# Kernel tuning notes

Hardware: AMD Instinct MI355X
Metric: run time of the kernel (lower is better)

Reference implementation:

```python
import jax, jax.numpy as jnp
import numpy as np

B, T, C, I = 4, 4096, 1024, 4096

def rmsnorm(x, w, eps=1e-6):
    return x * jax.lax.rsqrt(jnp.mean(x * x, axis=-1, keepdims=True) + eps) * w

def shift(h):
    # prepend zeros, drop last timestep: (B,T,C)
    return jnp.pad(h, ((0, 0), (1, 0), (0, 0)))[:, :-1]

def wkv_scan(k, v, w, u):
    # k, v: (B,T,C) fp32; w, u: (C,)
    ew = jnp.exp(jnp.clip(w, -20.0, 20.0))
    def step(carry, kv):
        a, b = carry
        kt, vt = kv  # (B,C)
        ekt = jnp.exp(jnp.clip(u + kt, -20.0, 20.0))
        out = (a + ekt * vt) / (b + ekt + 1e-8)
        ek = jnp.exp(jnp.clip(kt, -20.0, 20.0))
        return (ew * a + ek * vt, ew * b + ek), out
    init = (jnp.zeros((k.shape[0], k.shape[2]), jnp.float32),
            jnp.zeros((k.shape[0], k.shape[2]), jnp.float32))
    _, out = jax.lax.scan(step, init, (k.swapaxes(0, 1), v.swapaxes(0, 1)))
    return out.swapaxes(0, 1)  # (B,T,C)

def setup_inputs() -> dict:
    key = jax.random.key(0)
    ks = jax.random.split(key, 16)
    s = 1.0 / np.sqrt(C)
    si = 1.0 / np.sqrt(I)
    return {
        "x": jax.random.normal(ks[0], (B, T, C), jnp.float32),
        "ln1_w": jnp.ones((C,), jnp.float32),
        "ln2_w": jnp.ones((C,), jnp.float32),
        "time_decay": jax.random.normal(ks[1], (C,), jnp.float32) * 0.1 - 5.0,
        "time_first": jax.random.normal(ks[2], (C,), jnp.float32) * 0.01,
        "time_mix_k": jnp.full((C,), 0.5, jnp.float32),
        "time_mix_v": jnp.full((C,), 0.5, jnp.float32),
        "time_mix_r": jnp.full((C,), 0.5, jnp.float32),
        "W_key": jax.random.normal(ks[3], (C, C), jnp.float32) * s,
        "W_value": jax.random.normal(ks[4], (C, C), jnp.float32) * s,
        "W_recept": jax.random.normal(ks[5], (C, C), jnp.float32) * s,
        "W_out": jax.random.normal(ks[6], (C, C), jnp.float32) * s,
        "time_mix_k2": jnp.full((C,), 0.5, jnp.float32),
        "time_mix_r2": jnp.full((C,), 0.5, jnp.float32),
        "W_key2": jax.random.normal(ks[7], (C, I), jnp.float32) * s,
        "W_value2": jax.random.normal(ks[8], (I, C), jnp.float32) * si,
        "W_recept2": jax.random.normal(ks[9], (C, C), jnp.float32) * s,
    }

def reference(x, ln1_w, ln2_w, time_decay, time_first,
              time_mix_k, time_mix_v, time_mix_r,
              W_key, W_value, W_recept, W_out,
              time_mix_k2, time_mix_r2, W_key2, W_value2, W_recept2):
    # --- time mixing ---
    h = rmsnorm(x, ln1_w)
    sh = shift(h)
    xk = h * time_mix_k + sh * (1 - time_mix_k)
    xv = h * time_mix_v + sh * (1 - time_mix_v)
    xr = h * time_mix_r + sh * (1 - time_mix_r)
    k = xk @ W_key
    v = xv @ W_value
    r = jax.nn.sigmoid(xr @ W_recept)
    w = -jnp.exp(time_decay)
    u = time_first
    wkv = wkv_scan(k.astype(jnp.float32), v.astype(jnp.float32), w, u).astype(x.dtype)
    x = x + (r * wkv) @ W_out
    # --- channel mixing ---
    h = rmsnorm(x, ln2_w)
    sh = shift(h)
    xk = h * time_mix_k2 + sh * (1 - time_mix_k2)
    xr = h * time_mix_r2 + sh * (1 - time_mix_r2)
    k2 = jnp.square(jax.nn.relu(xk @ W_key2))
    r2 = jax.nn.sigmoid(xr @ W_recept2)
    return x + r2 * (k2 @ W_value2)
```

## Files before the change

kernel.cpp:

```cpp
#include <hip/hip_runtime.h>
#include <cstdint>
#include <cstddef>

#define B_ 4
#define T_ 4096
#define C_ 1024
#define I_ 4096
#define M_ (B_*T_)

__device__ __forceinline__ float bf2f(uint16_t u) {
    union { uint32_t i; float f; } v; v.i = ((uint32_t)u) << 16; return v.f;
}
__device__ __forceinline__ uint16_t f2bf(float f) {
    union { float f; uint32_t i; } v; v.f = f;
    uint32_t i = v.i;
    return (uint16_t)((i + 0x7fffu + ((i >> 16) & 1u)) >> 16);
}

typedef __bf16 bf16x8 __attribute__((ext_vector_type(8)));
typedef float  f32x4  __attribute__((ext_vector_type(4)));

__device__ __forceinline__ void async16(const void* g, void* l) {
    __builtin_amdgcn_global_load_lds(
        (const __attribute__((address_space(1))) void*)g,
        (__attribute__((address_space(3))) void*)l, 16, 0, 0);
}

__global__ void sniff_kernel(const uint32_t* __restrict__ w,
                             int* __restrict__ flag, int* __restrict__ one) {
    *flag = (w[0] == 0x3F003F00u) ? 1 : 0;
    *one = 1;
}

struct VecPtrs { const void* s[9]; uint16_t* d[9]; };
__global__ __launch_bounds__(256) void convert_vecs(VecPtrs p, const int* __restrict__ flagp) {
    const int f = *flagp;
    const int tid = threadIdx.x;
    for (int a = 0; a < 9; ++a) {
        const void* s = p.s[a]; uint16_t* d = p.d[a];
        for (int i = tid; i < C_; i += 256)
            d[i] = f ? ((const uint16_t*)s)[i] : f2bf(((const float*)s)[i]);
    }
}

struct TJobs { const void* src[7]; uint16_t* dst[7]; };
__global__ __launch_bounds__(256) void transpose_all(TJobs tj, const int* __restrict__ flagp)
{
    __shared__ uint16_t tile[64][65];
    const int f = *flagp;
    const int bid = blockIdx.x;
    int w, t, R, Cc, cx, cy;
    if (bid < 1280) {
        w = bid >> 8; t = bid & 255; R = C_; Cc = C_; cx = t & 15; cy = t >> 4;
    } else if (bid < 2304) {
        w = 5; t = bid - 1280; R = C_; Cc = I_; cx = t & 63; cy = t >> 6;
    } else {
        w = 6; t = bid - 2304; R = I_; Cc = C_; cx = t & 15; cy = t >> 4;
    }
    const void* in = tj.src[w];
    uint16_t* out = tj.dst[w];
    const int lc = threadIdx.x & 63;
    const int rg = threadIdx.x >> 6;
    const int c0 = cx * 64, r0 = cy * 64;
    #pragma unroll
    for (int i = 0; i < 16; ++i) {
        int lr = rg * 16 + i;
        size_t idx = (size_t)(r0 + lr) * Cc + c0 + lc;
        tile[lr][lc] = f ? ((const uint16_t*)in)[idx] : f2bf(((const float*)in)[idx]);
    }
    __syncthreads();
    #pragma unroll
    for (int i = 0; i < 16; ++i) {
        int lcc = rg * 16 + i;
        out[(size_t)(c0 + lcc) * R + r0 + lc] = tile[lc][lcc];
    }
}

__global__ __launch_bounds__(256) void mix_kernel(
    const void* __restrict__ x, const uint16_t* __restrict__ ln,
    const uint16_t* __restrict__ mk, const uint16_t* __restrict__ mv,
    const uint16_t* __restrict__ mr, const int* __restrict__ flagp,
    uint16_t* __restrict__ xk, uint16_t* __restrict__ xv, uint16_t* __restrict__ xr)
{
    const int row = blockIdx.x;
    const int tid = threadIdx.x;
    const int f = *flagp;
    const bool hasPrev = (row & (T_ - 1)) != 0;
    const size_t base = (size_t)row * C_;

    float c[4], p[4];
    if (f) {
        const uint16_t* xb = (const uint16_t*)x;
        uint2 cu = ((const uint2*)(xb + base))[tid];
        uint2 pu; pu.x = 0u; pu.y = 0u;
        if (hasPrev) pu = ((const uint2*)(xb + base - C_))[tid];
        c[0] = bf2f((uint16_t)(cu.x & 0xffff)); c[1] = bf2f((uint16_t)(cu.x >> 16));
        c[2] = bf2f((uint16_t)(cu.y & 0xffff)); c[3] = bf2f((uint16_t)(cu.y >> 16));
        p[0] = bf2f((uint16_t)(pu.x & 0xffff)); p[1] = bf2f((uint16_t)(pu.x >> 16));
        p[2] = bf2f((uint16_t)(pu.y & 0xffff)); p[3] = bf2f((uint16_t)(pu.y >> 16));
    } else {
        const float* xf = (const float*)x;
        float4 cf = ((const float4*)(xf + base))[tid];
        float4 pf; pf.x = pf.y = pf.z = pf.w = 0.f;
        if (hasPrev) pf = ((const float4*)(xf + base - C_))[tid];
        c[0] = cf.x; c[1] = cf.y; c[2] = cf.z; c[3] = cf.w;
        p[0] = pf.x; p[1] = pf.y; p[2] = pf.z; p[3] = pf.w;
    }

    float s1 = c[0]*c[0] + c[1]*c[1] + c[2]*c[2] + c[3]*c[3];
    float s2 = p[0]*p[0] + p[1]*p[1] + p[2]*p[2] + p[3]*p[3];
    #pragma unroll
    for (int off = 32; off > 0; off >>= 1) {
        s1 += __shfl_down(s1, off);
        s2 += __shfl_down(s2, off);
    }
    __shared__ float red[8];
    const int lane = tid & 63, wave = tid >> 6;
    if (lane == 0) { red[wave * 2] = s1; red[wave * 2 + 1] = s2; }
    __syncthreads();
    s1 = red[0] + red[2] + red[4] + red[6];
    s2 = red[1] + red[3] + red[5] + red[7];
    const float rs1 = rsqrtf(s1 * (1.f / C_) + 1e-6f);
    const float rs2 = rsqrtf(s2 * (1.f / C_) + 1e-6f);

    uint2 lnu = ((const uint2*)ln)[tid];
    uint2 mku = ((const uint2*)mk)[tid];
    uint2 mru = ((const uint2*)mr)[tid];
    float lnv[4] = { bf2f((uint16_t)(lnu.x & 0xffff)), bf2f((uint16_t)(lnu.x >> 16)),
                     bf2f((uint16_t)(lnu.y & 0xffff)), bf2f((uint16_t)(lnu.y >> 16)) };
    float mkv[4] = { bf2f((uint16_t)(mku.x & 0xffff)), bf2f((uint16_t)(mku.x >> 16)),
                     bf2f((uint16_t)(mku.y & 0xffff)), bf2f((uint16_t)(mku.y >> 16)) };
    float mrv[4] = { bf2f((uint16_t)(mru.x & 0xffff)), bf2f((uint16_t)(mru.x >> 16)),
                     bf2f((uint16_t)(mru.y & 0xffff)), bf2f((uint16_t)(mru.y >> 16)) };

    float h[4], sh[4];
    #pragma unroll
    for (int e = 0; e < 4; ++e) {
        h[e]  = c[e] * rs1 * lnv[e];
        sh[e] = p[e] * rs2 * lnv[e];
    }

    uint16_t ok[4], orr[4];
    #pragma unroll
    for (int e = 0; e < 4; ++e) {
        ok[e]  = f2bf(h[e] * mkv[e] + sh[e] * (1.f - mkv[e]));
        orr[e] = f2bf(h[e] * mrv[e] + sh[e] * (1.f - mrv[e]));
    }
    uint2 w;
    w.x = (uint32_t)ok[0] | ((uint32_t)ok[1] << 16);  w.y = (uint32_t)ok[2] | ((uint32_t)ok[3] << 16);
    ((uint2*)(xk + base))[tid] = w;
    w.x = (uint32_t)orr[0] | ((uint32_t)orr[1] << 16); w.y = (uint32_t)orr[2] | ((uint32_t)orr[3] << 16);
    ((uint2*)(xr + base))[tid] = w;

    if (xv != nullptr) {
        uint2 mvu = ((const uint2*)mv)[tid];
        float mvv[4] = { bf2f((uint16_t)(mvu.x & 0xffff)), bf2f((uint16_t)(mvu.x >> 16)),
                         bf2f((uint16_t)(mvu.y & 0xffff)), bf2f((uint16_t)(mvu.y >> 16)) };
        uint16_t ov[4];
        #pragma unroll
        for (int e = 0; e < 4; ++e)
            ov[e] = f2bf(h[e] * mvv[e] + sh[e] * (1.f - mvv[e]));
        w.x = (uint32_t)ov[0] | ((uint32_t)ov[1] << 16);  w.y = (uint32_t)ov[2] | ((uint32_t)ov[3] << 16);
        ((uint2*)(xv + base))[tid] = w;
    }
}

#define SCAN_L   64
#define SCAN_NCH (T_ / SCAN_L)

__global__ __launch_bounds__(256) void wkv_pass1(
    const uint16_t* __restrict__ kb, const uint16_t* __restrict__ vb,
    const uint16_t* __restrict__ td,
    float* __restrict__ sumA, float* __restrict__ sumB)
{
    const int gid = blockIdx.x * 256 + threadIdx.x;
    const int c = gid & (C_ - 1);
    const int j = (gid >> 10) & (SCAN_NCH - 1);
    const int b = gid >> 16;
    float w = -__expf(bf2f(td[c]));
    w = fminf(fmaxf(w, -20.f), 20.f);
    const float ew = __expf(w);
    const size_t base = ((size_t)(b * T_ + j * SCAN_L)) * C_ + c;
    float A = 0.f, Bs = 0.f;
    #pragma unroll 8
    for (int i = 0; i < SCAN_L; ++i) {
        float kt = bf2f(kb[base + (size_t)i * C_]);
        float vt = bf2f(vb[base + (size_t)i * C_]);
        float ek = __expf(fminf(fmaxf(kt, -20.f), 20.f));
        A  = ew * A  + ek * vt;
        Bs = ew * Bs + ek;
    }
    const size_t sidx = ((size_t)(b * SCAN_NCH + j)) * C_ + c;
    sumA[sidx] = A; sumB[sidx] = Bs;
}

__global__ __launch_bounds__(256) void wkv_pass2(
    const float* __restrict__ sumA, const float* __restrict__ sumB,
    const uint16_t* __restrict__ td,
    float* __restrict__ a0s, float* __restrict__ b0s)
{
    const int gid = blockIdx.x * 256 + threadIdx.x;
    const int c = gid & (C_ - 1);
    const int b = gid >> 10;
    float w = -__expf(bf2f(td[c]));
    w = fminf(fmaxf(w, -20.f), 20.f);
    const float dL = __expf(w * (float)SCAN_L);
    float a = 0.f, bs = 0.f;
    for (int j = 0; j < SCAN_NCH; ++j) {
        size_t idx = ((size_t)(b * SCAN_NCH + j)) * C_ + c;
        a0s[idx] = a; b0s[idx] = bs;
        a  = dL * a  + sumA[idx];
        bs = dL * bs + sumB[idx];
    }
}

__global__ __launch_bounds__(256) void wkv_pass3(
    const uint16_t* __restrict__ kb, const uint16_t* __restrict__ vb,
    const uint16_t* __restrict__ rb, const uint16_t* __restrict__ td,
    const uint16_t* __restrict__ tf,
    const float* __restrict__ a0s, const float* __restrict__ b0s,
    uint16_t* __restrict__ rwkv)
{
    const int gid = blockIdx.x * 256 + threadIdx.x;
    const int c = gid & (C_ - 1);
    const int j = (gid >> 10) & (SCAN_NCH - 1);
    const int b = gid >> 16;
    float w = -__expf(bf2f(td[c]));
    w = fminf(fmaxf(w, -20.f), 20.f);
    const float ew = __expf(w);
    const float u = bf2f(tf[c]);
    const size_t base = ((size_t)(b * T_ + j * SCAN_L)) * C_ + c;
    const size_t sidx = ((size_t)(b * SCAN_NCH + j)) * C_ + c;
    float a = a0s[sidx], bs = b0s[sidx];
    #pragma unroll 4
    for (int i = 0; i < SCAN_L; ++i) {
        float kt = bf2f(kb[base + (size_t)i * C_]);
        float vt = bf2f(vb[base + (size_t)i * C_]);
        float rt = bf2f(rb[base + (size_t)i * C_]);
        float eu = __expf(fminf(fmaxf(u + kt, -20.f), 20.f));
        float out = __fdividef(a + eu * vt, bs + eu + 1e-8f);
        rwkv[base + (size_t)i * C_] = f2bf(rt * out);
        float ek = __expf(fminf(fmaxf(kt, -20.f), 20.f));
        a  = ew * a  + ek * vt;
        bs = ew * bs + ek;
    }
}

struct GJob {
    const uint16_t* A; const uint16_t* BT; void* Out;
    const void* aux1; const uint16_t* aux2;
    int mode; int N; int K;
};
struct GJobs { GJob j[3]; };

#define EP_PITCH 72
#define EP_QUAD  4608

__global__ __launch_bounds__(256) void gemm_rt(GJobs js, const int* __restrict__ flagp)
{
    __shared__ uint16_t smem[18432];
    uint16_t* sA = smem;
    uint16_t* sB = smem + 8192;

    const GJob jb = js.j[blockIdx.z];
    const int N = jb.N, K = jb.K, mode = jb.mode;
    const int tid = threadIdx.x;
    const int lane = tid & 63, wave = tid >> 6;
    const int wr = wave >> 1, wc = wave & 1;
    const int laneM = lane & 15, quad = lane >> 4;

    const int pid = blockIdx.y * gridDim.x + blockIdx.x;
    const int group_size = 16 * gridDim.x;
    const int grp = pid / group_size;
    const int sub = pid - grp * group_size;
    const int pm = grp * 16 + (sub & 15);
    const int pn = sub >> 4;
    if (pn * 128 >= N) return;
    const int tileM = pm * 128, tileN = pn * 128;

    int f = 1;
    if (mode == 2 || mode == 4) f = *flagp;

    f32x4 acc[4][4];
    #pragma unroll
    for (int i = 0; i < 4; ++i)
        #pragma unroll
        for (int j = 0; j < 4; ++j)
            acc[i][j] = (f32x4){0.f, 0.f, 0.f, 0.f};

    const uint16_t* Abase = jb.A  + (size_t)tileM * K;
    const uint16_t* Bbase = jb.BT + (size_t)tileN * K;

    int srow[4], scol[4];
    #pragma unroll
    for (int it = 0; it < 4; ++it) {
        int g = it * 256 + tid;
        srow[it] = g >> 3;
        scol[it] = ((g & 7) ^ (srow[it] & 7)) * 8;
    }
    const int swz = laneM & 7;

    for (int kt = 0; kt < K; kt += 64) {
        #pragma unroll
        for (int it = 0; it < 4; ++it)
            async16(Abase + (size_t)srow[it] * K + kt + scol[it], &sA[(it * 256 + tid) * 8]);
        #pragma unroll
        for (int it = 0; it < 4; ++it)
            async16(Bbase + (size_t)srow[it] * K + kt + scol[it], &sB[(it * 256 + tid) * 8]);
        __syncthreads();
        #pragma unroll
        for (int h = 0; h < 2; ++h) {
            bf16x8 av[4], bv[4];
            const int gk = (h * 4 + quad) ^ swz;
            #pragma unroll
            for (int i = 0; i < 4; ++i) {
                av[i] = *(const bf16x8*)&sA[(wr * 64 + i * 16 + laneM) * 64 + gk * 8];
                bv[i] = *(const bf16x8*)&sB[(wc * 64 + i * 16 + laneM) * 64 + gk * 8];
            }
            #pragma unroll
            for (int i = 0; i < 4; ++i)
                #pragma unroll
                for (int j = 0; j < 4; ++j)
                    acc[i][j] = __builtin_amdgcn_mfma_f32_16x16x32_bf16(av[i], bv[j], acc[i][j], 0, 0, 0);
        }
        __syncthreads();
    }

    const int qbase = (wr * 2 + wc) * EP_QUAD;
    #pragma unroll
    for (int i = 0; i < 4; ++i) {
        #pragma unroll
        for (int j = 0; j < 4; ++j) {
            #pragma unroll
            for (int rr = 0; rr < 4; ++rr) {
                float v = acc[i][j][rr];
                if (mode == 1) v = __fdividef(1.f, 1.f + __expf(-v));
                else if (mode == 3) { float t = fmaxf(v, 0.f); v = t * t; }
                int row_l = i * 16 + quad * 4 + rr;
                int col_l = j * 16 + laneM;
                smem[qbase + row_l * EP_PITCH + col_l] = f2bf(v);
            }
        }
    }
    __syncthreads();

    #pragma unroll
    for (int s = 0; s < 8; ++s) {
        int segid = s * 256 + tid;
        int gr = segid >> 4;
        int c0 = (segid & 15) * 8;
        int lidx = ((gr >> 6) * 2 + (c0 >> 6)) * EP_QUAD + (gr & 63) * EP_PITCH + (c0 & 63);
        uint4 pk = *(const uint4*)&smem[lidx];
        size_t idx = (size_t)(tileM + gr) * N + tileN + c0;

        if (mode == 0 || mode == 1 || mode == 3) {
            *(uint4*)((uint16_t*)jb.Out + idx) = pk;
        } else {
            union { uint4 u; uint16_t h[8]; } P; P.u = pk;
            float vals[8];
            #pragma unroll
            for (int e = 0; e < 8; ++e) vals[e] = bf2f(P.h[e]);
            if (mode == 2) {
                float xres[8];
                if (f) {
                    union { uint4 u; uint16_t h[8]; } A1;
                    A1.u = *(const uint4*)((const uint16_t*)jb.aux1 + idx);
                    #pragma unroll
                    for (int e = 0; e < 8; ++e) xres[e] = bf2f(A1.h[e]);
                } else {
                    const float* af = (const float*)jb.aux1 + idx;
                    float4 a0 = *(const float4*)af;
                    float4 a1 = *(const float4*)(af + 4);
                    xres[0]=a0.x; xres[1]=a0.y; xres[2]=a0.z; xres[3]=a0.w;
                    xres[4]=a1.x; xres[5]=a1.y; xres[6]=a1.z; xres[7]=a1.w;
                }
                union { uint4 u; uint16_t h[8]; } O;
                #pragma unroll
                for (int e = 0; e < 8; ++e) O.h[e] = f2bf(vals[e] + xres[e]);
                *(uint4*)((uint16_t*)jb.Out + idx) = O.u;
            } else {
                union { uint4 u; uint16_t h[8]; } A1, A2;
                A1.u = *(const uint4*)((const uint16_t*)jb.aux1 + idx);
                A2.u = *(const uint4*)(jb.aux2 + idx);
                float res[8];
                #pragma unroll
                for (int e = 0; e < 8; ++e)
                    res[e] = bf2f(A1.h[e]) + bf2f(A2.h[e]) * vals[e];
                if (f) {
                    union { uint4 u; uint16_t h[8]; } O;
                    #pragma unroll
                    for (int e = 0; e < 8; ++e) O.h[e] = f2bf(res[e]);
                    *(uint4*)((uint16_t*)jb.Out + idx) = O.u;
                } else {
                    float* of = (float*)jb.Out + idx;
                    *(float4*)of       = (float4){res[0], res[1], res[2], res[3]};
                    *(float4*)(of + 4) = (float4){res[4], res[5], res[6], res[7]};
                }
            }
        }
    }
}

extern "C" void kernel_launch(void* const* d_in, const int* in_sizes, int n_in,
                              void* d_out, int out_size, void* d_ws, size_t ws_size,
                              hipStream_t stream)
{
    const void* x   = d_in[0];
    const void* ln1 = d_in[1];
    const void* ln2 = d_in[2];
    const void* td  = d_in[3];
    const void* tf  = d_in[4];
    const void* mk  = d_in[5];
    const void* mv  = d_in[6];
    const void* mr  = d_in[7];
    const void* Wk  = d_in[8];
    const void* Wv  = d_in[9];
    const void* Wr  = d_in[10];
    const void* Wo  = d_in[11];
    const void* mk2 = d_in[12];
    const void* mr2 = d_in[13];
    const void* Wk2 = d_in[14];
    const void* Wv2 = d_in[15];
    const void* Wr2 = d_in[16];

    char* ws = (char*)d_ws;
    const size_t MiB = 1u << 20;
    uint16_t* WkT  = (uint16_t*)(ws + 0 * MiB);
    uint16_t* WvT  = (uint16_t*)(ws + 2 * MiB);
    uint16_t* WrT  = (uint16_t*)(ws + 4 * MiB);
    uint16_t* WoT  = (uint16_t*)(ws + 6 * MiB);
    uint16_t* Wr2T = (uint16_t*)(ws + 8 * MiB);
    uint16_t* Wk2T = (uint16_t*)(ws + 10 * MiB);
    uint16_t* Wv2T = (uint16_t*)(ws + 18 * MiB);
    uint16_t* A0 = (uint16_t*)(ws + 26 * MiB);
    uint16_t* A1 = (uint16_t*)(ws + 58 * MiB);
    uint16_t* A2 = (uint16_t*)(ws + 90 * MiB);
    uint16_t* A3 = (uint16_t*)(ws + 122 * MiB);
    uint16_t* A4 = (uint16_t*)(ws + 154 * MiB);
    uint16_t* A5 = (uint16_t*)(ws + 186 * MiB);
    uint16_t* k2 = (uint16_t*)(ws + 122 * MiB);
    float* sumA = (float*)(ws + 58 * MiB);
    float* sumB = (float*)(ws + 59 * MiB);
    float* a0s  = (float*)(ws + 60 * MiB);
    float* b0s  = (float*)(ws + 61 * MiB);
    int* flagp = (int*)(ws + 250 * MiB);
    int* onep  = (int*)(ws + 250 * MiB + 16);
    uint16_t* vecs = (uint16_t*)(ws + 250 * MiB + 64);
    uint16_t* ln1c = vecs + 0 * C_;
    uint16_t* ln2c = vecs + 1 * C_;
    uint16_t* tdc  = vecs + 2 * C_;
    uint16_t* tfc  = vecs + 3 * C_;
    uint16_t* mkc  = vecs + 4 * C_;
    uint16_t* mvc  = vecs + 5 * C_;
    uint16_t* mrc  = vecs + 6 * C_;
    uint16_t* mk2c = vecs + 7 * C_;
    uint16_t* mr2c = vecs + 8 * C_;

    uint16_t* xk   = A0;
    uint16_t* xv   = A1;
    uint16_t* xr   = A2;
    uint16_t* kb   = A3;
    uint16_t* vb   = A4;
    uint16_t* rb   = A5;
    uint16_t* rwkv = A0;
    uint16_t* x2   = A1;
    uint16_t* xk2  = A2;
    uint16_t* xr2  = A3;
    uint16_t* r2   = A0;

    dim3 blk(256);

    sniff_kernel<<<1, 1, 0, stream>>>((const uint32_t*)mk, flagp, onep);
    VecPtrs vp;
    vp.s[0] = ln1; vp.s[1] = ln2; vp.s[2] = td;  vp.s[3] = tf;  vp.s[4] = mk;
    vp.s[5] = mv;  vp.s[6] = mr;  vp.s[7] = mk2; vp.s[8] = mr2;
    vp.d[0] = ln1c; vp.d[1] = ln2c; vp.d[2] = tdc;  vp.d[3] = tfc;  vp.d[4] = mkc;
    vp.d[5] = mvc;  vp.d[6] = mrc;  vp.d[7] = mk2c; vp.d[8] = mr2c;
    convert_vecs<<<1, blk, 0, stream>>>(vp, flagp);

    TJobs tj;
    tj.src[0] = Wk;  tj.dst[0] = WkT;
    tj.src[1] = Wv;  tj.dst[1] = WvT;
    tj.src[2] = Wr;  tj.dst[2] = WrT;
    tj.src[3] = Wo;  tj.dst[3] = WoT;
    tj.src[4] = Wr2; tj.dst[4] = Wr2T;
    tj.src[5] = Wk2; tj.dst[5] = Wk2T;
    tj.src[6] = Wv2; tj.dst[6] = Wv2T;
    transpose_all<<<3328, blk, 0, stream>>>(tj, flagp);

    mix_kernel<<<M_, blk, 0, stream>>>(x, ln1c, mkc, mvc, mrc, flagp, xk, xv, xr);

    GJobs kvr;
    kvr.j[0] = GJob{ xk, WkT, kb, nullptr, nullptr, 0, C_, C_ };
    kvr.j[1] = GJob{ xv, WvT, vb, nullptr, nullptr, 0, C_, C_ };
    kvr.j[2] = GJob{ xr, WrT, rb, nullptr, nullptr, 1, C_, C_ };
    gemm_rt<<<dim3(C_ / 128, M_ / 128, 3), blk, 0, stream>>>(kvr, flagp);

    wkv_pass1<<<(B_ * SCAN_NCH * C_) / 256, blk, 0, stream>>>(kb, vb, tdc, sumA, sumB);
    wkv_pass2<<<(B_ * C_) / 256, blk, 0, stream>>>(sumA, sumB, tdc, a0s, b0s);
    wkv_pass3<<<(B_ * SCAN_NCH * C_) / 256, blk, 0, stream>>>(kb, vb, rb, tdc, tfc, a0s, b0s, rwkv);

    GJobs g2; g2.j[0] = GJob{ rwkv, WoT, x2, x, nullptr, 2, C_, C_ };
    g2.j[1] = g2.j[0]; g2.j[2] = g2.j[0];
    gemm_rt<<<dim3(C_ / 128, M_ / 128, 1), blk, 0, stream>>>(g2, flagp);

    mix_kernel<<<M_, blk, 0, stream>>>(x2, ln2c, mk2c, nullptr, mr2c, onep, xk2, nullptr, xr2);

    GJobs g3;
    g3.j[0] = GJob{ xr2, Wr2T, r2, nullptr, nullptr, 1, C_, C_ };
    g3.j[1] = GJob{ xk2, Wk2T, k2, nullptr, nullptr, 3, I_, C_ };
    g3.j[2] = g3.j[0];
    gemm_rt<<<dim3(I_ / 128, M_ / 128, 2), blk, 0, stream>>>(g3, flagp);

    GJobs g4; g4.j[0] = GJob{ k2, Wv2T, d_out, x2, r2, 4, C_, I_ };
    g4.j[1] = g4.j[0]; g4.j[2] = g4.j[0];
    gemm_rt<<<dim3(C_ / 128, M_ / 128, 1), blk, 0, stream>>>(g4, flagp);

    (void)in_sizes; (void)n_in; (void)out_size; (void)ws_size;
}
```

Measured before the change: 955.5 us.

## Fuse receptance GEMM and sigmoid into final value GEMM epilogue

```diff
diff --git a/kernel.cpp b/kernel.cpp
--- a/kernel.cpp
+++ b/kernel.cpp
@@ -248,7 +248,7 @@
 
 struct GJob {
     const uint16_t* A; const uint16_t* BT; void* Out;
-    const void* aux1; const uint16_t* aux2;
+    const void* aux1;
     int mode; int N; int K;
 };
 struct GJobs { GJob j[3]; };
@@ -279,7 +279,7 @@
     const int tileM = pm * 128, tileN = pn * 128;
 
     int f = 1;
-    if (mode == 2 || mode == 4) f = *flagp;
+    if (mode == 2) f = *flagp;
 
     f32x4 acc[4][4];
     #pragma unroll
@@ -336,9 +336,7 @@
                 float v = acc[i][j][rr];
                 if (mode == 1) v = __fdividef(1.f, 1.f + __expf(-v));
                 else if (mode == 3) { float t = fmaxf(v, 0.f); v = t * t; }
-                int row_l = i * 16 + quad * 4 + rr;
-                int col_l = j * 16 + laneM;
-                smem[qbase + row_l * EP_PITCH + col_l] = f2bf(v);
+                smem[qbase + (i * 16 + quad * 4 + rr) * EP_PITCH + j * 16 + laneM] = f2bf(v);
             }
         }
     }
@@ -353,50 +351,185 @@
         uint4 pk = *(const uint4*)&smem[lidx];
         size_t idx = (size_t)(tileM + gr) * N + tileN + c0;
 
-        if (mode == 0 || mode == 1 || mode == 3) {
+        if (mode != 2) {
             *(uint4*)((uint16_t*)jb.Out + idx) = pk;
         } else {
             union { uint4 u; uint16_t h[8]; } P; P.u = pk;
-            float vals[8];
-            #pragma unroll
-            for (int e = 0; e < 8; ++e) vals[e] = bf2f(P.h[e]);
-            if (mode == 2) {
-                float xres[8];
-                if (f) {
-                    union { uint4 u; uint16_t h[8]; } A1;
-                    A1.u = *(const uint4*)((const uint16_t*)jb.aux1 + idx);
+            float xres[8];
+            if (f) {
+                union { uint4 u; uint16_t h[8]; } A1;
+                A1.u = *(const uint4*)((const uint16_t*)jb.aux1 + idx);
+                #pragma unroll
+                for (int e = 0; e < 8; ++e) xres[e] = bf2f(A1.h[e]);
+            } else {
+                const float* af = (const float*)jb.aux1 + idx;
+                float4 a0 = *(const float4*)af;
+                float4 a1 = *(const float4*)(af + 4);
+                xres[0]=a0.x; xres[1]=a0.y; xres[2]=a0.z; xres[3]=a0.w;
+                xres[4]=a1.x; xres[5]=a1.y; xres[6]=a1.z; xres[7]=a1.w;
+            }
+            union { uint4 u; uint16_t h[8]; } O;
+            #pragma unroll
+            for (int e = 0; e < 8; ++e) O.h[e] = f2bf(bf2f(P.h[e]) + xres[e]);
+            *(uint4*)((uint16_t*)jb.Out + idx) = O.u;
+        }
+    }
+}
+
+__global__ __launch_bounds__(256) void gemm_fused(
+    const uint16_t* __restrict__ Ar, const uint16_t* __restrict__ BTr, int K2,
+    const uint16_t* __restrict__ Ak, const uint16_t* __restrict__ BTk, int K,
+    const uint16_t* __restrict__ x2, void* __restrict__ Out,
+    const int* __restrict__ flagp)
+{
+    __shared__ uint16_t smem[18432];
+    uint16_t* sA = smem;
+    uint16_t* sB = smem + 8192;
+
+    const int N = C_;
+    const int tid = threadIdx.x;
+    const int lane = tid & 63, wave = tid >> 6;
+    const int wr = wave >> 1, wc = wave & 1;
+    const int laneM = lane & 15, quad = lane >> 4;
+
+    const int pid = blockIdx.y * gridDim.x + blockIdx.x;
+    const int group_size = 16 * gridDim.x;
+    const int grp = pid / group_size;
+    const int sub = pid - grp * group_size;
+    const int pm = grp * 16 + (sub & 15);
+    const int pn = sub >> 4;
+    const int tileM = pm * 128, tileN = pn * 128;
+
+    const int f = *flagp;
+
+    int srow[4], scol[4];
+    #pragma unroll
+    for (int it = 0; it < 4; ++it) {
+        int g = it * 256 + tid;
+        srow[it] = g >> 3;
+        scol[it] = ((g & 7) ^ (srow[it] & 7)) * 8;
+    }
+    const int swz = laneM & 7;
+
+    f32x4 acc[4][4];
+    #pragma unroll
+    for (int i = 0; i < 4; ++i)
+        #pragma unroll
+        for (int j = 0; j < 4; ++j)
+            acc[i][j] = (f32x4){0.f, 0.f, 0.f, 0.f};
+
+    {
+        const uint16_t* Abase = Ar  + (size_t)tileM * K2;
+        const uint16_t* Bbase = BTr + (size_t)tileN * K2;
+        for (int kt = 0; kt < K2; kt += 64) {
+            #pragma unroll
+            for (int it = 0; it < 4; ++it)
+                async16(Abase + (size_t)srow[it] * K2 + kt + scol[it], &sA[(it * 256 + tid) * 8]);
+            #pragma unroll
+            for (int it = 0; it < 4; ++it)
+                async16(Bbase + (size_t)srow[it] * K2 + kt + scol[it], &sB[(it * 256 + tid) * 8]);
+            __syncthreads();
+            #pragma unroll
+            for (int h = 0; h < 2; ++h) {
+                bf16x8 av[4], bv[4];
+                const int gk = (h * 4 + quad) ^ swz;
+                #pragma unroll
+                for (int i = 0; i < 4; ++i) {
+                    av[i] = *(const bf16x8*)&sA[(wr * 64 + i * 16 + laneM) * 64 + gk * 8];
+                    bv[i] = *(const bf16x8*)&sB[(wc * 64 + i * 16 + laneM) * 64 + gk * 8];
+                }
+                #pragma unroll
+                for (int i = 0; i < 4; ++i)
                     #pragma unroll
-                    for (int e = 0; e < 8; ++e) xres[e] = bf2f(A1.h[e]);
-                } else {
-                    const float* af = (const float*)jb.aux1 + idx;
-                    float4 a0 = *(const float4*)af;
-                    float4 a1 = *(const float4*)(af + 4);
-                    xres[0]=a0.x; xres[1]=a0.y; xres[2]=a0.z; xres[3]=a0.w;
-                    xres[4]=a1.x; xres[5]=a1.y; xres[6]=a1.z; xres[7]=a1.w;
+                    for (int j = 0; j < 4; ++j)
+                        acc[i][j] = __builtin_amdgcn_mfma_f32_16x16x32_bf16(av[i], bv[j], acc[i][j], 0, 0, 0);
+            }
+            __syncthreads();
+        }
+    }
+
+    uint32_t r2p[4][4][2];
+    #pragma unroll
+    for (int i = 0; i < 4; ++i)
+        #pragma unroll
+        for (int j = 0; j < 4; ++j) {
+            uint16_t h0 = f2bf(__fdividef(1.f, 1.f + __expf(-acc[i][j][0])));
+            uint16_t h1 = f2bf(__fdividef(1.f, 1.f + __expf(-acc[i][j][1])));
+            uint16_t h2 = f2bf(__fdividef(1.f, 1.f + __expf(-acc[i][j][2])));
+            uint16_t h3 = f2bf(__fdividef(1.f, 1.f + __expf(-acc[i][j][3])));
+            r2p[i][j][0] = (uint32_t)h0 | ((uint32_t)h1 << 16);
+            r2p[i][j][1] = (uint32_t)h2 | ((uint32_t)h3 << 16);
+            acc[i][j] = (f32x4){0.f, 0.f, 0.f, 0.f};
+        }
+
+    {
+        const uint16_t* Abase = Ak  + (size_t)tileM * K;
+        const uint16_t* Bbase = BTk + (size_t)tileN * K;
+        for (int kt = 0; kt < K; kt += 64) {
+            #pragma unroll
+            for (int it = 0; it < 4; ++it)
+                async16(Abase + (size_t)srow[it] * K + kt + scol[it], &sA[(it * 256 + tid) * 8]);
+            #pragma unroll
+            for (int it = 0; it < 4; ++it)
+                async16(Bbase + (size_t)srow[it] * K + kt + scol[it], &sB[(it * 256 + tid) * 8]);
+            __syncthreads();
+            #pragma unroll
+            for (int h = 0; h < 2; ++h) {
+                bf16x8 av[4], bv[4];
+                const int gk = (h * 4 + quad) ^ swz;
+                #pragma unroll
+                for (int i = 0; i < 4; ++i) {
+                    av[i] = *(const bf16x8*)&sA[(wr * 64 + i * 16 + laneM) * 64 + gk * 8];
+                    bv[i] = *(const bf16x8*)&sB[(wc * 64 + i * 16 + laneM) * 64 + gk * 8];
                 }
-                union { uint4 u; uint16_t h[8]; } O;
                 #pragma unroll
-                for (int e = 0; e < 8; ++e) O.h[e] = f2bf(vals[e] + xres[e]);
-                *(uint4*)((uint16_t*)jb.Out + idx) = O.u;
-            } else {
-                union { uint4 u; uint16_t h[8]; } A1, A2;
-                A1.u = *(const uint4*)((const uint16_t*)jb.aux1 + idx);
-                A2.u = *(const uint4*)(jb.aux2 + idx);
-                float res[8];
-                #pragma unroll
-                for (int e = 0; e < 8; ++e)
-                    res[e] = bf2f(A1.h[e]) + bf2f(A2.h[e]) * vals[e];
-                if (f) {
-                    union { uint4 u; uint16_t h[8]; } O;
+                for (int i = 0; i < 4; ++i)
                     #pragma unroll
-                    for (int e = 0; e < 8; ++e) O.h[e] = f2bf(res[e]);
-                    *(uint4*)((uint16_t*)jb.Out + idx) = O.u;
-                } else {
-                    float* of = (float*)jb.Out + idx;
-                    *(float4*)of       = (float4){res[0], res[1], res[2], res[3]};
-                    *(float4*)(of + 4) = (float4){res[4], res[5], res[6], res[7]};
-                }
+                    for (int j = 0; j < 4; ++j)
+                        acc[i][j] = __builtin_amdgcn_mfma_f32_16x16x32_bf16(av[i], bv[j], acc[i][j], 0, 0, 0);
             }
+            __syncthreads();
+        }
+    }
+
+    const int qbase = (wr * 2 + wc) * EP_QUAD;
+    #pragma unroll
+    for (int i = 0; i < 4; ++i) {
+        #pragma unroll
+        for (int j = 0; j < 4; ++j) {
+            #pragma unroll
+            for (int rr = 0; rr < 4; ++rr) {
+                uint16_t rh = (uint16_t)(r2p[i][j][rr >> 1] >> ((rr & 1) * 16));
+                float v = bf2f(rh) * acc[i][j][rr];
+                smem[qbase + (i * 16 + quad * 4 + rr) * EP_PITCH + j * 16 + laneM] = f2bf(v);
+            }
+        }
+    }
+    __syncthreads();
+
+    #pragma unroll
+    for (int s = 0; s < 8; ++s) {
+        int segid = s * 256 + tid;
+        int gr = segid >> 4;
+        int c0 = (segid & 15) * 8;
+        int lidx = ((gr >> 6) * 2 + (c0 >> 6)) * EP_QUAD + (gr & 63) * EP_PITCH + (c0 & 63);
+        union { uint4 u; uint16_t h[8]; } P;
+        P.u = *(const uint4*)&smem[lidx];
+        size_t idx = (size_t)(tileM + gr) * N + tileN + c0;
+        union { uint4 u; uint16_t h[8]; } X;
+        X.u = *(const uint4*)(x2 + idx);
+        float res[8];
+        #pragma unroll
+        for (int e = 0; e < 8; ++e) res[e] = bf2f(X.h[e]) + bf2f(P.h[e]);
+        if (f) {
+            union { uint4 u; uint16_t h[8]; } O;
+            #pragma unroll
+            for (int e = 0; e < 8; ++e) O.h[e] = f2bf(res[e]);
+            *(uint4*)((uint16_t*)Out + idx) = O.u;
+        } else {
+            float* of = (float*)Out + idx;
+            *(float4*)of       = (float4){res[0], res[1], res[2], res[3]};
+            *(float4*)(of + 4) = (float4){res[4], res[5], res[6], res[7]};
         }
     }
 }
@@ -465,8 +598,7 @@
     uint16_t* rwkv = A0;
     uint16_t* x2   = A1;
     uint16_t* xk2  = A2;
-    uint16_t* xr2  = A3;
-    uint16_t* r2   = A0;
+    uint16_t* xr2  = A0;
 
     dim3 blk(256);
 
@@ -491,30 +623,27 @@
     mix_kernel<<<M_, blk, 0, stream>>>(x, ln1c, mkc, mvc, mrc, flagp, xk, xv, xr);
 
     GJobs kvr;
-    kvr.j[0] = GJob{ xk, WkT, kb, nullptr, nullptr, 0, C_, C_ };
-    kvr.j[1] = GJob{ xv, WvT, vb, nullptr, nullptr, 0, C_, C_ };
-    kvr.j[2] = GJob{ xr, WrT, rb, nullptr, nullptr, 1, C_, C_ };
+    kvr.j[0] = GJob{ xk, WkT, kb, nullptr, 0, C_, C_ };
+    kvr.j[1] = GJob{ xv, WvT, vb, nullptr, 0, C_, C_ };
+    kvr.j[2] = GJob{ xr, WrT, rb, nullptr, 1, C_, C_ };
     gemm_rt<<<dim3(C_ / 128, M_ / 128, 3), blk, 0, stream>>>(kvr, flagp);
 
     wkv_pass1<<<(B_ * SCAN_NCH * C_) / 256, blk, 0, stream>>>(kb, vb, tdc, sumA, sumB);
     wkv_pass2<<<(B_ * C_) / 256, blk, 0, stream>>>(sumA, sumB, tdc, a0s, b0s);
     wkv_pass3<<<(B_ * SCAN_NCH * C_) / 256, blk, 0, stream>>>(kb, vb, rb, tdc, tfc, a0s, b0s, rwkv);
 
-    GJobs g2; g2.j[0] = GJob{ rwkv, WoT, x2, x, nullptr, 2, C_, C_ };
+    GJobs g2; g2.j[0] = GJob{ rwkv, WoT, x2, x, 2, C_, C_ };
     g2.j[1] = g2.j[0]; g2.j[2] = g2.j[0];
     gemm_rt<<<dim3(C_ / 128, M_ / 128, 1), blk, 0, stream>>>(g2, flagp);
 
     mix_kernel<<<M_, blk, 0, stream>>>(x2, ln2c, mk2c, nullptr, mr2c, onep, xk2, nullptr, xr2);
 
-    GJobs g3;
-    g3.j[0] = GJob{ xr2, Wr2T, r2, nullptr, nullptr, 1, C_, C_ };
-    g3.j[1] = GJob{ xk2, Wk2T, k2, nullptr, nullptr, 3, I_, C_ };
-    g3.j[2] = g3.j[0];
-    gemm_rt<<<dim3(I_ / 128, M_ / 128, 2), blk, 0, stream>>>(g3, flagp);
-
-    GJobs g4; g4.j[0] = GJob{ k2, Wv2T, d_out, x2, r2, 4, C_, I_ };
-    g4.j[1] = g4.j[0]; g4.j[2] = g4.j[0];
-    gemm_rt<<<dim3(C_ / 128, M_ / 128, 1), blk, 0, stream>>>(g4, flagp);
+    GJobs g3; g3.j[0] = GJob{ xk2, Wk2T, k2, nullptr, 3, I_, C_ };
+    g3.j[1] = g3.j[0]; g3.j[2] = g3.j[0];
+    gemm_rt<<<dim3(I_ / 128, M_ / 128, 1), blk, 0, stream>>>(g3, flagp);
+
+    gemm_fused<<<dim3(C_ / 128, M_ / 128), blk, 0, stream>>>(
+        xr2, Wr2T, C_, k2, Wv2T, I_, x2, d_out, flagp);
 
     (void)in_sizes; (void)n_in; (void)out_size; (void)ws_size;
 }
```

After: 950.2 us. Within noise of the previous version (-0.6%).
